# Kernel tuning notes

Hardware: AMD Instinct MI355X
Metric: run time of the kernel (lower is better)

Reference implementation:

```python
import jax, jax.numpy as jnp
import numpy as np
import math

EMB, HEAD, B, S = 1024, 64, 4, 4096

def setup_inputs() -> dict:
    key = jax.random.key(0)
    ks = jax.random.split(key, 7)
    scale = 1.0 / math.sqrt(EMB)
    return {
        "x": jax.random.normal(ks[0], (B, S, EMB), dtype=jnp.float32),
        "Wq": jax.random.uniform(ks[1], (EMB, HEAD), jnp.float32, -scale, scale),
        "bq": jax.random.uniform(ks[2], (HEAD,), jnp.float32, -scale, scale),
        "Wk": jax.random.uniform(ks[3], (EMB, HEAD), jnp.float32, -scale, scale),
        "bk": jax.random.uniform(ks[4], (HEAD,), jnp.float32, -scale, scale),
        "Wv": jax.random.uniform(ks[5], (EMB, HEAD), jnp.float32, -scale, scale),
        "bv": jax.random.uniform(ks[6], (HEAD,), jnp.float32, -scale, scale),
    }

def reference(x, Wq, bq, Wk, bk, Wv, bv):
    # x: [B, S, E]
    q = x @ Wq + bq            # [B, S, H]
    k = x @ Wk + bk
    v = x @ Wv + bv
    scores = jnp.einsum('bqh,bkh->bqk', q, k) / math.sqrt(q.shape[-1])
    # causal mask: position q attends to k <= q
    s = x.shape[1]
    causal = jnp.tril(jnp.ones((s, s), dtype=bool))
    scores = jnp.where(causal, scores, -jnp.inf)
    attn = jax.nn.softmax(scores, axis=-1)
    return jnp.einsum('bqk,bkh->bqh', attn, v)
```

## Files before the change

kernel.cpp:

```cpp
#include <hip/hip_runtime.h>
#include <hip/hip_bf16.h>
#include <math.h>

#define EMB 1024
#define HEAD 64
#define NB 4
#define SEQ 4096
#define MTOT (NB * SEQ)
#define QSCALE (0.125f * 1.44269504088896f)
#define MBOUND 4.0f

typedef __attribute__((ext_vector_type(8))) short bf16x8;
typedef __attribute__((ext_vector_type(4))) float f32x4;
typedef __attribute__((ext_vector_type(16))) float f32x16;
typedef __attribute__((ext_vector_type(2))) unsigned u32x2;

static __device__ __forceinline__ unsigned short f2b(float f) {
    union { float f; unsigned u; } v; v.f = f;
    unsigned r = v.u + 0x7FFFu + ((v.u >> 16) & 1u);
    return (unsigned short)(r >> 16);
}
static __device__ __forceinline__ float b2f(unsigned short u) {
    union { unsigned u; float f; } v; v.u = ((unsigned)u) << 16; return v.f;
}
static __device__ __forceinline__ unsigned pk2(float lo, float hi) {
    unsigned r;
    asm("v_cvt_pk_bf16_f32 %0, %1, %2" : "=v"(r) : "v"(lo), "v"(hi));
    return r;
}
static __device__ __forceinline__ float ex2(float x) {
    float r;
    asm("v_exp_f32 %0, %1" : "=v"(r) : "v"(x));
    return r;
}

__global__ void wb_kernel(const float* __restrict__ Wq, const float* __restrict__ Wk,
                          const float* __restrict__ Wv, unsigned short* __restrict__ Wb) {
    const int f = blockIdx.x % 12, ks = blockIdx.x / 12;
    const int t = threadIdx.x;
    const int h = t >> 7, lane = (t >> 1) & 63, j0 = (t & 1) * 4;
    const int li = lane & 15, lg = lane >> 4;
    const float* W = (f < 4) ? Wq : (f < 8) ? Wk : Wv;
    const int nc = (f & 3) * 16 + li;
    const int k0 = ks * 64 + h * 32 + lg * 8 + j0;
    const unsigned u0 = pk2(W[(size_t)(k0 + 0) * HEAD + nc], W[(size_t)(k0 + 1) * HEAD + nc]);
    const unsigned u1 = pk2(W[(size_t)(k0 + 2) * HEAD + nc], W[(size_t)(k0 + 3) * HEAD + nc]);
    unsigned short* dst = Wb + (size_t)(f * 16 + ks) * 1024 + h * 512 + lane * 8 + j0;
    *(u32x2*)dst = (u32x2){u0, u1};
}

__global__ __launch_bounds__(256) void proj_kernel(
    const float* __restrict__ x, const unsigned short* __restrict__ Wb,
    const float* __restrict__ bq, const float* __restrict__ bk,
    const float* __restrict__ bv, unsigned short* __restrict__ qb,
    unsigned short* __restrict__ kb, unsigned short* __restrict__ vb) {
    __shared__ unsigned short Xl[16][1032];

    const int tid = threadIdx.x;
    const int nh = tid >> 6, lane = tid & 63;
    const int li = lane & 15, lg = lane >> 4;
    const int rbase = blockIdx.x * 16;

    {
        const int row = tid >> 4, cf = (tid & 15) * 8;
        const float* xr = x + (size_t)(rbase + row) * EMB;
#pragma unroll
        for (int j = 0; j < 8; ++j) {
            const int col = j * 128 + cf;
            const float4 t0 = *(const float4*)(xr + col);
            const float4 t1 = *(const float4*)(xr + col + 4);
            union { bf16x8 v; unsigned u[4]; } pa;
            pa.u[0] = pk2(t0.x, t0.y); pa.u[1] = pk2(t0.z, t0.w);
            pa.u[2] = pk2(t1.x, t1.y); pa.u[3] = pk2(t1.z, t1.w);
            *(bf16x8*)&Xl[row][col] = pa.v;
        }
    }
    __syncthreads();

    f32x4 acc[3];
#pragma unroll
    for (int n = 0; n < 3; ++n) acc[n] = (f32x4){0.f, 0.f, 0.f, 0.f};

    bf16x8 wA[3][2], wB[3][2];
#pragma unroll
    for (int n = 0; n < 3; ++n) {
        const unsigned short* wp = Wb + (size_t)((nh * 3 + n) * 16 + 0) * 1024 + lane * 8;
        wA[n][0] = *(const bf16x8*)(wp);
        wA[n][1] = *(const bf16x8*)(wp + 512);
    }
#pragma unroll
    for (int ks = 0; ks < 16; ++ks) {
        if (ks < 15) {
#pragma unroll
            for (int n = 0; n < 3; ++n) {
                const unsigned short* wp = Wb + (size_t)((nh * 3 + n) * 16 + ks + 1) * 1024 + lane * 8;
                if (ks & 1) { wA[n][0] = *(const bf16x8*)(wp); wA[n][1] = *(const bf16x8*)(wp + 512); }
                else        { wB[n][0] = *(const bf16x8*)(wp); wB[n][1] = *(const bf16x8*)(wp + 512); }
            }
        }
        const bf16x8 a0 = *(const bf16x8*)&Xl[li][ks * 64 + lg * 8];
        const bf16x8 a1 = *(const bf16x8*)&Xl[li][ks * 64 + 32 + lg * 8];
#pragma unroll
        for (int n = 0; n < 3; ++n) {
            const int f = nh * 3 + n;
            const bf16x8 b0 = (ks & 1) ? wB[n][0] : wA[n][0];
            const bf16x8 b1 = (ks & 1) ? wB[n][1] : wA[n][1];
            if (f < 8) {
                acc[n] = __builtin_amdgcn_mfma_f32_16x16x32_bf16(b0, a0, acc[n], 0, 0, 0);
                acc[n] = __builtin_amdgcn_mfma_f32_16x16x32_bf16(b1, a1, acc[n], 0, 0, 0);
            } else {
                acc[n] = __builtin_amdgcn_mfma_f32_16x16x32_bf16(a0, b0, acc[n], 0, 0, 0);
                acc[n] = __builtin_amdgcn_mfma_f32_16x16x32_bf16(a1, b1, acc[n], 0, 0, 0);
            }
        }
    }

    const int si0 = rbase & 4095, bi = rbase >> 12;
#pragma unroll
    for (int n = 0; n < 3; ++n) {
        const int f = nh * 3 + n;
        if (f < 8) {
            const float* bias = (f < 4) ? bq : bk;
            const int dbase = (f & 3) * 16 + lg * 4;
            const float4 bb = *(const float4*)&bias[dbase];
            const float qs = (f < 4) ? QSCALE : 1.0f;
            unsigned short* dst = (f < 4) ? qb : kb;
            const size_t plane = (size_t)((bi * 2 + (lg >> 1)) * 4 + (f & 3)) * (SEQ * 8);
            const unsigned u0 = pk2((acc[n][0] + bb.x) * qs, (acc[n][1] + bb.y) * qs);
            const unsigned u1 = pk2((acc[n][2] + bb.z) * qs, (acc[n][3] + bb.w) * qs);
            unsigned short* p = dst + plane + (size_t)(si0 + li) * 8 + (lg & 1) * 4;
            *(u32x2*)p = (u32x2){u0, u1};
        } else {
            const int nc = (f & 3) * 16 + li;
            const float bb = bv[nc];
            const unsigned u0 = pk2(acc[n][0] + bb, acc[n][1] + bb);
            const unsigned u1 = pk2(acc[n][2] + bb, acc[n][3] + bb);
            const int si = si0 + lg * 4;
            unsigned short* p = vb + ((size_t)bi * 512 + (si >> 3)) * 512 + nc * 8 + (si & 7);
            *(u32x2*)p = (u32x2){u0, u1};
        }
    }
}

template<int W64, int NWIN, int KMAX>
__global__ __launch_bounds__(64) void attn_kernel(
    const unsigned short* __restrict__ Qb, const unsigned short* __restrict__ Kb,
    const unsigned short* __restrict__ Vb, unsigned* __restrict__ pO,
    float* __restrict__ pL) {
    const int lane = threadIdx.x & 63;
    const int ql = lane & 31, h = lane >> 5;
    const int b = blockIdx.y;
    const int w = blockIdx.x;
    int seg = 0;
#pragma unroll
    for (int kk = 1; kk < KMAX; ++kk)
        if (w >= 128 * kk - W64 * kk * (kk - 1)) seg = kk;
    const int Os = 128 * seg - W64 * seg * (seg - 1);
    const int qidx = 2 * W64 * seg + (w - Os);
    const int tdiag = qidx >> 1;
    const int qa0 = qidx * 32;
    const int t0 = W64 * seg;
    const int tend = (t0 + W64 < tdiag + 1) ? t0 + W64 : tdiag + 1;

    const unsigned short* qb0 = Qb + ((size_t)(b * 2 + h)) * 4 * (SEQ * 8);
    const unsigned short* kb0 = Kb + ((size_t)(b * 2 + h)) * 4 * (SEQ * 8);
    const unsigned short* vb0 = Vb + (size_t)b * 512 * 512;

    bf16x8 qf[4];
#pragma unroll
    for (int s = 0; s < 4; ++s)
        qf[s] = *(const bf16x8*)(qb0 + (size_t)s * (SEQ * 8) + (size_t)(qa0 + ql) * 8);

    f32x16 oa0, oa1;
#pragma unroll
    for (int r = 0; r < 16; ++r) { oa0[r] = 0.f; oa1[r] = 0.f; }
    float lsum = 0.f;

    bf16x8 kcur[2][4], knxt[2][4];
#pragma unroll
    for (int hh = 0; hh < 2; ++hh)
#pragma unroll
        for (int s = 0; s < 4; ++s)
            kcur[hh][s] = *(const bf16x8*)(kb0 + (size_t)s * (SEQ * 8)
                                           + ((size_t)t0 * 64 + 32 * hh + ql) * 8);

    for (int t = t0; t < tend; ++t) {
        bf16x8 vf[2][4];
#pragma unroll
        for (int dt = 0; dt < 2; ++dt)
#pragma unroll
            for (int cc = 0; cc < 4; ++cc)
                vf[dt][cc] = *(const bf16x8*)(vb0 + ((size_t)t * 8 + 2 * cc + h) * 512
                                              + (dt * 32 + ql) * 8);
        if (t + 1 < tend) {
#pragma unroll
            for (int hh = 0; hh < 2; ++hh)
#pragma unroll
                for (int s = 0; s < 4; ++s)
                    knxt[hh][s] = *(const bf16x8*)(kb0 + (size_t)s * (SEQ * 8)
                                                   + ((size_t)(t + 1) * 64 + 32 * hh + ql) * 8);
        }

        f32x16 st0, st1;
#pragma unroll
        for (int r = 0; r < 16; ++r) { st0[r] = 0.f; st1[r] = 0.f; }
        __builtin_amdgcn_s_setprio(1);
#pragma unroll
        for (int s = 0; s < 4; ++s) {
            st0 = __builtin_amdgcn_mfma_f32_32x32x16_bf16(kcur[0][s], qf[s], st0, 0, 0, 0);
            st1 = __builtin_amdgcn_mfma_f32_32x32x16_bf16(kcur[1][s], qf[s], st1, 0, 0, 0);
        }
        __builtin_amdgcn_s_setprio(0);

        if (t == tdiag) {
            if (qidx & 1) {
#pragma unroll
                for (int r = 0; r < 16; ++r) {
                    const int kvl = (r & 3) + 8 * (r >> 2) + 4 * h;
                    if (kvl > ql) st1[r] = -1e30f;
                }
            } else {
#pragma unroll
                for (int r = 0; r < 16; ++r) {
                    const int kvl = (r & 3) + 8 * (r >> 2) + 4 * h;
                    if (kvl > ql) st0[r] = -1e30f;
                    st1[r] = -1e30f;
                }
            }
        }
#pragma unroll
        for (int r = 0; r < 16; ++r) {
            st0[r] = ex2(st0[r] - MBOUND);
            st1[r] = ex2(st1[r] - MBOUND);
        }
        {
            float q0 = (st0[0] + st0[1]) + (st0[2] + st0[3]);
            float q1 = (st0[4] + st0[5]) + (st0[6] + st0[7]);
            float q2 = (st0[8] + st0[9]) + (st0[10] + st0[11]);
            float q3 = (st0[12] + st0[13]) + (st0[14] + st0[15]);
            float q4 = (st1[0] + st1[1]) + (st1[2] + st1[3]);
            float q5 = (st1[4] + st1[5]) + (st1[6] + st1[7]);
            float q6 = (st1[8] + st1[9]) + (st1[10] + st1[11]);
            float q7 = (st1[12] + st1[13]) + (st1[14] + st1[15]);
            lsum += ((q0 + q1) + (q2 + q3)) + ((q4 + q5) + (q6 + q7));
        }

        bf16x8 bfv[4];
#pragma unroll
        for (int hh = 0; hh < 2; ++hh) {
            unsigned w8[8];
#pragma unroll
            for (int tt = 0; tt < 8; ++tt)
                w8[tt] = hh ? pk2(st1[2 * tt], st1[2 * tt + 1])
                            : pk2(st0[2 * tt], st0[2 * tt + 1]);
            const unsigned xa0 = h ? w8[0] : w8[2];
            const unsigned va0 = __shfl_xor((int)xa0, 32);
            const unsigned xb0 = h ? w8[1] : w8[3];
            const unsigned vb_0 = __shfl_xor((int)xb0, 32);
            union { bf16x8 v; unsigned u[4]; } bbv;
            bbv.u[0] = h ? va0 : w8[0];
            bbv.u[1] = h ? vb_0 : w8[1];
            bbv.u[2] = h ? w8[2] : va0;
            bbv.u[3] = h ? w8[3] : vb_0;
            bfv[hh * 2] = bbv.v;
            const unsigned xa1 = h ? w8[4] : w8[6];
            const unsigned va1 = __shfl_xor((int)xa1, 32);
            const unsigned xb1 = h ? w8[5] : w8[7];
            const unsigned vb_1 = __shfl_xor((int)xb1, 32);
            bbv.u[0] = h ? va1 : w8[4];
            bbv.u[1] = h ? vb_1 : w8[5];
            bbv.u[2] = h ? w8[6] : va1;
            bbv.u[3] = h ? w8[7] : vb_1;
            bfv[hh * 2 + 1] = bbv.v;
        }
        __builtin_amdgcn_s_setprio(1);
#pragma unroll
        for (int cc = 0; cc < 4; ++cc) {
            oa0 = __builtin_amdgcn_mfma_f32_32x32x16_bf16(vf[0][cc], bfv[cc], oa0, 0, 0, 0);
            oa1 = __builtin_amdgcn_mfma_f32_32x32x16_bf16(vf[1][cc], bfv[cc], oa1, 0, 0, 0);
        }
        __builtin_amdgcn_s_setprio(0);

#pragma unroll
        for (int hh = 0; hh < 2; ++hh)
#pragma unroll
            for (int s = 0; s < 4; ++s)
                kcur[hh][s] = knxt[hh][s];
    }

    lsum += __shfl_xor(lsum, 32);
    const size_t gw = (size_t)b * NWIN + w;
    unsigned* po = pO + gw * 1024;
#pragma unroll
    for (int r = 0; r < 16; r += 2) {
        const int dp = ((r & 3) >> 1) + 4 * (r >> 2) + 2 * h;
        po[dp * 32 + ql] = pk2(oa0[r], oa0[r + 1]);
        po[(16 + dp) * 32 + ql] = pk2(oa1[r], oa1[r + 1]);
    }
    if (h == 0) pL[gw * 32 + ql] = lsum;
}

template<int W64, int NWIN>
__global__ __launch_bounds__(256) void merge_kernel(
    const unsigned* __restrict__ pO, const float* __restrict__ pL,
    float* __restrict__ out) {
    const int qidx = blockIdx.x, b = blockIdx.y;
    const int wcount = qidx / (2 * W64) + 1;
    const int t = threadIdx.x;
    const int ql = t & 31, g = t >> 5;

    float acc[8] = {0.f, 0.f, 0.f, 0.f, 0.f, 0.f, 0.f, 0.f};
    float L = 0.f;
    for (int k = 0; k < wcount; ++k) {
        const int Os = 128 * k - W64 * k * (k - 1);
        const size_t gw = (size_t)b * NWIN + Os + (qidx - 2 * W64 * k);
        L += pL[gw * 32 + ql];
#pragma unroll
        for (int i = 0; i < 4; ++i) {
            const unsigned u = pO[gw * 1024 + (size_t)(g * 4 + i) * 32 + ql];
            acc[2 * i] += b2f((unsigned short)(u & 0xFFFFu));
            acc[2 * i + 1] += b2f((unsigned short)(u >> 16));
        }
    }
    const float inv = 1.0f / L;
    float* op = out + ((size_t)b * SEQ + qidx * 32 + ql) * HEAD + g * 8;
    f32x4 o0 = {acc[0] * inv, acc[1] * inv, acc[2] * inv, acc[3] * inv};
    f32x4 o1 = {acc[4] * inv, acc[5] * inv, acc[6] * inv, acc[7] * inv};
    *(f32x4*)(op) = o0;
    *(f32x4*)(op + 4) = o1;
}

extern "C" void kernel_launch(void* const* d_in, const int* in_sizes, int n_in,
                              void* d_out, int out_size, void* d_ws, size_t ws_size,
                              hipStream_t stream) {
    const float* x  = (const float*)d_in[0];
    const float* Wq = (const float*)d_in[1];
    const float* bq = (const float*)d_in[2];
    const float* Wk = (const float*)d_in[3];
    const float* bk = (const float*)d_in[4];
    const float* Wv = (const float*)d_in[5];
    const float* bv = (const float*)d_in[6];

    unsigned short* Wb = (unsigned short*)d_ws;
    unsigned short* qb = Wb + 3 * HEAD * EMB;
    unsigned short* kb = qb + (size_t)MTOT * HEAD;
    unsigned short* vb = kb + (size_t)MTOT * HEAD;
    unsigned* pO = (unsigned*)(vb + (size_t)MTOT * HEAD);
    const size_t base_shorts = (size_t)3 * HEAD * EMB + (size_t)3 * MTOT * HEAD;

    wb_kernel<<<dim3(192), dim3(256), 0, stream>>>(Wq, Wk, Wv, Wb);
    proj_kernel<<<dim3(MTOT / 16), dim3(256), 0, stream>>>(x, Wb, bq, bk, bv, qb, kb, vb);

    const size_t need4 = base_shorts * 2 + (size_t)NB * 1088 * (1024 * 4 + 32 * 4);
    if (ws_size >= need4) {
        float* pL = (float*)(pO + (size_t)NB * 1088 * 1024);
        attn_kernel<4, 1088, 16><<<dim3(1088, NB), dim3(64), 0, stream>>>(qb, kb, vb, pO, pL);
        merge_kernel<4, 1088><<<dim3(128, NB), dim3(256), 0, stream>>>(pO, pL, (float*)d_out);
    } else {
        float* pL = (float*)(pO + (size_t)NB * 576 * 1024);
        attn_kernel<8, 576, 8><<<dim3(576, NB), dim3(64), 0, stream>>>(qb, kb, vb, pO, pL);
        merge_kernel<8, 576><<<dim3(128, NB), dim3(256), 0, stream>>>(pO, pL, (float*)d_out);
    }
}
```

Before: 62.26 us.

## Process two row tiles per projection block, prefetching the second during the first

The projection kernel now handles 32 rows per block in two 16-row tiles with double-buffered shared memory. The second tile's x loads are issued into registers before the first tile's MFMA loop, so global load latency overlaps with compute. It also halves the grid size. The cost is 64 extra VGPRs for the prefetched float4s and doubled LDS per block, which may reduce occupancy.

```diff
diff --git a/kernel.cpp b/kernel.cpp
--- a/kernel.cpp
+++ b/kernel.cpp
@@ -49,42 +49,14 @@
     *(u32x2*)dst = (u32x2){u0, u1};
 }
 
-__global__ __launch_bounds__(256) void proj_kernel(
-    const float* __restrict__ x, const unsigned short* __restrict__ Wb,
-    const float* __restrict__ bq, const float* __restrict__ bk,
-    const float* __restrict__ bv, unsigned short* __restrict__ qb,
-    unsigned short* __restrict__ kb, unsigned short* __restrict__ vb) {
-    __shared__ unsigned short Xl[16][1032];
-
-    const int tid = threadIdx.x;
-    const int nh = tid >> 6, lane = tid & 63;
-    const int li = lane & 15, lg = lane >> 4;
-    const int rbase = blockIdx.x * 16;
-
-    {
-        const int row = tid >> 4, cf = (tid & 15) * 8;
-        const float* xr = x + (size_t)(rbase + row) * EMB;
-#pragma unroll
-        for (int j = 0; j < 8; ++j) {
-            const int col = j * 128 + cf;
-            const float4 t0 = *(const float4*)(xr + col);
-            const float4 t1 = *(const float4*)(xr + col + 4);
-            union { bf16x8 v; unsigned u[4]; } pa;
-            pa.u[0] = pk2(t0.x, t0.y); pa.u[1] = pk2(t0.z, t0.w);
-            pa.u[2] = pk2(t1.x, t1.y); pa.u[3] = pk2(t1.z, t1.w);
-            *(bf16x8*)&Xl[row][col] = pa.v;
-        }
-    }
-    __syncthreads();
-
-    f32x4 acc[3];
-#pragma unroll
-    for (int n = 0; n < 3; ++n) acc[n] = (f32x4){0.f, 0.f, 0.f, 0.f};
-
+static __device__ __forceinline__ void proj_kloop(
+    const unsigned short* __restrict__ X,
+    const unsigned short* __restrict__ Wb,
+    int nh, int lane, int li, int lg, f32x4* acc) {
     bf16x8 wA[3][2], wB[3][2];
 #pragma unroll
     for (int n = 0; n < 3; ++n) {
-        const unsigned short* wp = Wb + (size_t)((nh * 3 + n) * 16 + 0) * 1024 + lane * 8;
+        const unsigned short* wp = Wb + (size_t)((nh * 3 + n) * 16) * 1024 + lane * 8;
         wA[n][0] = *(const bf16x8*)(wp);
         wA[n][1] = *(const bf16x8*)(wp + 512);
     }
@@ -98,8 +70,8 @@
                 else        { wB[n][0] = *(const bf16x8*)(wp); wB[n][1] = *(const bf16x8*)(wp + 512); }
             }
         }
-        const bf16x8 a0 = *(const bf16x8*)&Xl[li][ks * 64 + lg * 8];
-        const bf16x8 a1 = *(const bf16x8*)&Xl[li][ks * 64 + 32 + lg * 8];
+        const bf16x8 a0 = *(const bf16x8*)(X + li * 1032 + ks * 64 + lg * 8);
+        const bf16x8 a1 = *(const bf16x8*)(X + li * 1032 + ks * 64 + 32 + lg * 8);
 #pragma unroll
         for (int n = 0; n < 3; ++n) {
             const int f = nh * 3 + n;
@@ -114,7 +86,13 @@
             }
         }
     }
-
+}
+
+static __device__ __forceinline__ void proj_epilogue(
+    const f32x4* acc, int rbase, int nh, int li, int lg,
+    const float* __restrict__ bq, const float* __restrict__ bk,
+    const float* __restrict__ bv, unsigned short* __restrict__ qb,
+    unsigned short* __restrict__ kb, unsigned short* __restrict__ vb) {
     const int si0 = rbase & 4095, bi = rbase >> 12;
 #pragma unroll
     for (int n = 0; n < 3; ++n) {
@@ -140,6 +118,71 @@
             *(u32x2*)p = (u32x2){u0, u1};
         }
     }
+}
+
+__global__ __launch_bounds__(256) void proj_kernel(
+    const float* __restrict__ x, const unsigned short* __restrict__ Wb,
+    const float* __restrict__ bq, const float* __restrict__ bk,
+    const float* __restrict__ bv, unsigned short* __restrict__ qb,
+    unsigned short* __restrict__ kb, unsigned short* __restrict__ vb) {
+    __shared__ unsigned short Xl[2][16][1032];
+
+    const int tid = threadIdx.x;
+    const int nh = tid >> 6, lane = tid & 63;
+    const int li = lane & 15, lg = lane >> 4;
+    const int row = tid >> 4, cf = (tid & 15) * 8;
+    const int rbase0 = blockIdx.x * 32;
+
+    float4 xa[16];
+    {
+        const float* xr = x + (size_t)(rbase0 + row) * EMB;
+#pragma unroll
+        for (int j = 0; j < 8; ++j) {
+            xa[2 * j]     = *(const float4*)(xr + j * 128 + cf);
+            xa[2 * j + 1] = *(const float4*)(xr + j * 128 + cf + 4);
+        }
+#pragma unroll
+        for (int j = 0; j < 8; ++j) {
+            union { bf16x8 v; unsigned u[4]; } pa;
+            pa.u[0] = pk2(xa[2 * j].x, xa[2 * j].y);
+            pa.u[1] = pk2(xa[2 * j].z, xa[2 * j].w);
+            pa.u[2] = pk2(xa[2 * j + 1].x, xa[2 * j + 1].y);
+            pa.u[3] = pk2(xa[2 * j + 1].z, xa[2 * j + 1].w);
+            *(bf16x8*)&Xl[0][row][j * 128 + cf] = pa.v;
+        }
+    }
+    __syncthreads();
+
+    {
+        const float* xr = x + (size_t)(rbase0 + 16 + row) * EMB;
+#pragma unroll
+        for (int j = 0; j < 8; ++j) {
+            xa[2 * j]     = *(const float4*)(xr + j * 128 + cf);
+            xa[2 * j + 1] = *(const float4*)(xr + j * 128 + cf + 4);
+        }
+    }
+
+    f32x4 acc[3];
+#pragma unroll
+    for (int n = 0; n < 3; ++n) acc[n] = (f32x4){0.f, 0.f, 0.f, 0.f};
+    proj_kloop(&Xl[0][0][0], Wb, nh, lane, li, lg, acc);
+
+#pragma unroll
+    for (int j = 0; j < 8; ++j) {
+        union { bf16x8 v; unsigned u[4]; } pa;
+        pa.u[0] = pk2(xa[2 * j].x, xa[2 * j].y);
+        pa.u[1] = pk2(xa[2 * j].z, xa[2 * j].w);
+        pa.u[2] = pk2(xa[2 * j + 1].x, xa[2 * j + 1].y);
+        pa.u[3] = pk2(xa[2 * j + 1].z, xa[2 * j + 1].w);
+        *(bf16x8*)&Xl[1][row][j * 128 + cf] = pa.v;
+    }
+    proj_epilogue(acc, rbase0, nh, li, lg, bq, bk, bv, qb, kb, vb);
+    __syncthreads();
+
+#pragma unroll
+    for (int n = 0; n < 3; ++n) acc[n] = (f32x4){0.f, 0.f, 0.f, 0.f};
+    proj_kloop(&Xl[1][0][0], Wb, nh, lane, li, lg, acc);
+    proj_epilogue(acc, rbase0 + 16, nh, li, lg, bq, bk, bv, qb, kb, vb);
 }
 
 template<int W64, int NWIN, int KMAX>
@@ -349,7 +392,7 @@
     const size_t base_shorts = (size_t)3 * HEAD * EMB + (size_t)3 * MTOT * HEAD;
 
     wb_kernel<<<dim3(192), dim3(256), 0, stream>>>(Wq, Wk, Wv, Wb);
-    proj_kernel<<<dim3(MTOT / 16), dim3(256), 0, stream>>>(x, Wb, bq, bk, bv, qb, kb, vb);
+    proj_kernel<<<dim3(MTOT / 32), dim3(256), 0, stream>>>(x, Wb, bq, bk, bv, qb, kb, vb);
 
     const size_t need4 = base_shorts * 2 + (size_t)NB * 1088 * (1024 * 4 + 32 * 4);
     if (ws_size >= need4) {
```

New measurement: 61.97 us. About the same (-0.5%).
